# Performance work log

Measured on AMD Instinct MI355X. Metric: run time of the kernel, lower is better.

## Reference

```python
import jax, jax.numpy as jnp
import numpy as np


def setup_inputs() -> dict:
    key = jax.random.key(0)
    k1, k2, k3, k4 = jax.random.split(key, 4)
    d_in, d_out = 1024, 1024
    x = jax.random.normal(k1, (4, 2048, d_in), dtype=jnp.float32)
    # nn.Linear weights, stored as [d_in, d_out] for x @ W (torch stores transpose)
    s = 1.0 / np.sqrt(d_in)
    Wq = jax.random.normal(k2, (d_in, d_out), dtype=jnp.float32) * s
    Wk = jax.random.normal(k3, (d_in, d_out), dtype=jnp.float32) * s
    Wv = jax.random.normal(k4, (d_in, d_out), dtype=jnp.float32) * s
    return {"x": x, "Wq": Wq, "Wk": Wk, "Wv": Wv}


def reference(x, Wq, Wk, Wv):
    # x: [b, s, d_in]; projections (no bias)
    q = jnp.einsum('bsi,io->bso', x, Wq)
    k = jnp.einsum('bsi,io->bso', x, Wk)
    v = jnp.einsum('bsi,io->bso', x, Wv)
    d_out = k.shape[-1]
    scores = jnp.einsum('bqd,bkd->bqk', q, k) / jnp.sqrt(jnp.float32(d_out))
    seq_len = x.shape[1]
    causal = jnp.tril(jnp.ones((seq_len, seq_len), dtype=bool))  # [s, s]
    scores = jnp.where(causal[None, :, :], scores, -jnp.inf)
    weights = jax.nn.softmax(scores, axis=-1)
    return jnp.einsum('bqk,bkd->bqd', weights, v)
```

## Files before the change

### kernel.cpp

```cpp
#include <hip/hip_runtime.h>

typedef __attribute__((ext_vector_type(8))) short bf16x8;
typedef __attribute__((ext_vector_type(4))) float f32x4;
typedef unsigned int u32;

__device__ __forceinline__ unsigned short f2bf(float f) {
  union { float f; unsigned int u; } a; a.f = f;
  unsigned int u = a.u;
  u += 0x7FFFu + ((u >> 16) & 1u);
  return (unsigned short)(u >> 16);
}
__device__ __forceinline__ float bf2f(unsigned short h) {
  union { unsigned int u; float f; } a; a.u = ((unsigned int)h) << 16;
  return a.f;
}

__device__ __forceinline__ void gload16(const unsigned short* g, unsigned short* l) {
  __builtin_amdgcn_global_load_lds((const __attribute__((address_space(1))) u32*)g,
                                   (__attribute__((address_space(3))) u32*)l, 16, 0, 0);
}

#define TM 128
#define TN 128
#define BK 64

template<int MODE>
__global__ __launch_bounds__(256, 4)
void gemm_bt(const unsigned short* __restrict__ A,
             const unsigned short* __restrict__ Bm,
             float* __restrict__ Cf,
             unsigned short* __restrict__ Cb,
             int K, long aBatch, long bBatch, long cBatch, float scale)
{
  int z = blockIdx.z;
  A  += (long)z * aBatch;
  Bm += (long)z * bBatch;
  if (MODE == 2) Cb += (long)z * cBatch;
  if (MODE == 3) Cf += (long)z * cBatch;

  int bm, bn;
  if (MODE == 2) {
    int f = blockIdx.x;
    int r = (int)((sqrtf((float)(8 * f + 1)) - 1.0f) * 0.5f);
    while ((r + 1) * (r + 2) / 2 <= f) r++;
    while (r * (r + 1) / 2 > f) r--;
    bm = r * TM;
    bn = (f - r * (r + 1) / 2) * TN;
  } else if (MODE == 3) {
    bm = (15 - blockIdx.y) * TM;
    bn = blockIdx.x * TN;
  } else {
    bm = blockIdx.y * TM;
    bn = blockIdx.x * TN;
  }
  int Keff = (MODE == 3) ? (bm + TM) : K;

  __shared__ __align__(16) unsigned short As[TM * BK];
  __shared__ __align__(16) unsigned short Bs[TN * BK];

  int tid  = threadIdx.x;
  int wave = tid >> 6, lane = tid & 63;
  int wm = (wave >> 1) * 64, wn = (wave & 1) * 64;
  int quad = lane >> 4, l16 = lane & 15;

  int r8 = lane >> 3;
  int c  = (lane & 7) ^ r8;
  int rs = wave * 32 + r8;
  const unsigned short* Ag = A  + (long)(bm + rs) * K + c * 8;
  const unsigned short* Bg = Bm + (long)(bn + rs) * K + c * 8;
  unsigned short* Al = &As[(wave * 32) * BK];
  unsigned short* Bl = &Bs[(wave * 32) * BK];

  f32x4 acc[4][4] = {};

  for (int k0 = 0; k0 < Keff; k0 += BK) {
#pragma unroll
    for (int g = 0; g < 4; g++) {
      gload16(Ag + k0 + (long)g * 8 * K, Al + g * 8 * BK);
      gload16(Bg + k0 + (long)g * 8 * K, Bl + g * 8 * BK);
    }
    __syncthreads();

#pragma unroll
    for (int h = 0; h < 2; h++) {
      bf16x8 af[4], bfr[4];
#pragma unroll
      for (int i = 0; i < 4; i++)
        af[i]  = *(const bf16x8*)&As[(wm + i * 16 + l16) * BK + (((quad + 4 * h) ^ (l16 & 7)) * 8)];
#pragma unroll
      for (int j = 0; j < 4; j++)
        bfr[j] = *(const bf16x8*)&Bs[(wn + j * 16 + l16) * BK + (((quad + 4 * h) ^ (l16 & 7)) * 8)];
#pragma unroll
      for (int i = 0; i < 4; i++)
#pragma unroll
        for (int j = 0; j < 4; j++)
          acc[i][j] = __builtin_amdgcn_mfma_f32_16x16x32_bf16(af[i], bfr[j], acc[i][j], 0, 0, 0);
    }
    __syncthreads();
  }

#pragma unroll
  for (int i = 0; i < 4; i++) {
    int grow0 = bm + wm + i * 16 + quad * 4;
#pragma unroll
    for (int j = 0; j < 4; j++) {
      int gcol = bn + wn + j * 16 + l16;
      if (MODE == 0) {
        int which = gcol >> 10;
        int col = gcol & 1023;
        if (which < 2) {
          unsigned short* dst = Cb + (long)which * 8192 * 1024;
#pragma unroll
          for (int r = 0; r < 4; r++)
            dst[(long)(grow0 + r) * 1024 + col] = f2bf(acc[i][j][r]);
        } else {
          unsigned short* Vt = Cb + (long)2 * 8192 * 1024;
          int bb = grow0 >> 11, s = grow0 & 2047;
          ushort4 pk;
          pk.x = f2bf(acc[i][j][0]); pk.y = f2bf(acc[i][j][1]);
          pk.z = f2bf(acc[i][j][2]); pk.w = f2bf(acc[i][j][3]);
          *(ushort4*)(Vt + ((long)bb * 1024 + col) * 2048 + s) = pk;
        }
      } else if (MODE == 2) {
#pragma unroll
        for (int r = 0; r < 4; r++)
          Cb[(long)(grow0 + r) * 2048 + gcol] = f2bf(acc[i][j][r] * scale);
      } else {
#pragma unroll
        for (int r = 0; r < 4; r++)
          Cf[(long)(grow0 + r) * 1024 + gcol] = acc[i][j][r];
      }
    }
  }
}

__global__ __launch_bounds__(256)
void cvt_bf16(const float* __restrict__ in, unsigned short* __restrict__ out, long n)
{
  long i = ((long)blockIdx.x * 256 + threadIdx.x) * 4;
  if (i >= n) return;
  float4 v = *(const float4*)(in + i);
  ushort4 o;
  o.x = f2bf(v.x); o.y = f2bf(v.y); o.z = f2bf(v.z); o.w = f2bf(v.w);
  *(ushort4*)(out + i) = o;
}

__global__ __launch_bounds__(256)
void trans_cvt(const float* __restrict__ W0, const float* __restrict__ W1, const float* __restrict__ W2,
               unsigned short* __restrict__ T0, unsigned short* __restrict__ T1, unsigned short* __restrict__ T2)
{
  int z = blockIdx.z;
  const float* W   = (z == 0) ? W0 : (z == 1) ? W1 : W2;
  unsigned short* T = (z == 0) ? T0 : (z == 1) ? T1 : T2;
  __shared__ float tile[32][33];
  int kb = blockIdx.x * 32, nb = blockIdx.y * 32;
  int tx = threadIdx.x & 31, ty = threadIdx.x >> 5;
  for (int r = ty; r < 32; r += 8)
    tile[r][tx] = W[(long)(kb + r) * 1024 + nb + tx];
  __syncthreads();
  for (int r = ty; r < 32; r += 8)
    T[(long)(nb + r) * 1024 + kb + tx] = f2bf(tile[tx][r]);
}

__global__ __launch_bounds__(256)
void softmax_rows(const unsigned short* __restrict__ Sc, unsigned short* __restrict__ P)
{
  int row = blockIdx.x, b = blockIdx.y;
  const unsigned short* Sr = Sc + ((long)b * 2048 + row) * 2048;
  unsigned short* Pr = P + ((long)b * 2048 + row) * 2048;
  int n = row + 1;
  int tid = threadIdx.x;
  int wave = tid >> 6, lane = tid & 63;
  __shared__ float sh[2048];
  __shared__ float red[4];

  float lmax = -1e30f;
  for (int j0 = tid * 4; j0 < n; j0 += 1024) {
    ushort4 rw = *(const ushort4*)(Sr + j0);
    float4 v;
    v.x = (j0 + 0 < n) ? bf2f(rw.x) : -1e30f;
    v.y = (j0 + 1 < n) ? bf2f(rw.y) : -1e30f;
    v.z = (j0 + 2 < n) ? bf2f(rw.z) : -1e30f;
    v.w = (j0 + 3 < n) ? bf2f(rw.w) : -1e30f;
    *(float4*)(sh + j0) = v;
    lmax = fmaxf(fmaxf(v.x, v.y), fmaxf(fmaxf(v.z, v.w), lmax));
  }
  for (int off = 32; off; off >>= 1) lmax = fmaxf(lmax, __shfl_down(lmax, off));
  if (lane == 0) red[wave] = lmax;
  __syncthreads();
  float rmax = fmaxf(fmaxf(red[0], red[1]), fmaxf(red[2], red[3]));
  __syncthreads();

  float lsum = 0.f;
  for (int j0 = tid * 4; j0 < n; j0 += 1024) {
    float4 v = *(const float4*)(sh + j0);
    v.x = __expf(v.x - rmax); v.y = __expf(v.y - rmax);
    v.z = __expf(v.z - rmax); v.w = __expf(v.w - rmax);
    *(float4*)(sh + j0) = v;
    lsum += v.x + v.y + v.z + v.w;
  }
  for (int off = 32; off; off >>= 1) lsum += __shfl_down(lsum, off);
  if (lane == 0) red[wave] = lsum;
  __syncthreads();
  float rinv = 1.0f / (red[0] + red[1] + red[2] + red[3]);

  int nW = (n + 255) & ~255;
  for (int j0 = tid * 4; j0 < nW; j0 += 1024) {
    ushort4 o;
    if (j0 + 3 < n) {
      float4 v = *(const float4*)(sh + j0);
      o.x = f2bf(v.x * rinv); o.y = f2bf(v.y * rinv);
      o.z = f2bf(v.z * rinv); o.w = f2bf(v.w * rinv);
    } else {
      float4 v = *(const float4*)(sh + j0);
      o.x = (j0 + 0 < n) ? f2bf(v.x * rinv) : (unsigned short)0;
      o.y = (j0 + 1 < n) ? f2bf(v.y * rinv) : (unsigned short)0;
      o.z = (j0 + 2 < n) ? f2bf(v.z * rinv) : (unsigned short)0;
      o.w = (j0 + 3 < n) ? f2bf(v.w * rinv) : (unsigned short)0;
    }
    *(ushort4*)(Pr + j0) = o;
  }
}

extern "C" void kernel_launch(void* const* d_in, const int* in_sizes, int n_in,
                              void* d_out, int out_size, void* d_ws, size_t ws_size,
                              hipStream_t stream) {
  const float* x  = (const float*)d_in[0];
  const float* Wq = (const float*)d_in[1];
  const float* Wk = (const float*)d_in[2];
  const float* Wv = (const float*)d_in[3];
  float* out = (float*)d_out;

  unsigned short* Xb  = (unsigned short*)d_ws;
  unsigned short* WqT = Xb  + (long)8192 * 1024;
  unsigned short* Q   = WqT + (long)3072 * 1024;
  unsigned short* Kb  = Q   + (long)8192 * 1024;
  unsigned short* Vt  = Kb  + (long)8192 * 1024;
  unsigned short* Sc  = Vt  + (long)8192 * 1024;
  unsigned short* P   = Sc  + (long)4 * 2048 * 2048;
  unsigned short* WkT = WqT + (long)1024 * 1024;
  unsigned short* WvT = WkT + (long)1024 * 1024;

  cvt_bf16<<<8192, 256, 0, stream>>>(x, Xb, (long)8388608);
  trans_cvt<<<dim3(32, 32, 3), 256, 0, stream>>>(Wq, Wk, Wv, WqT, WkT, WvT);

  gemm_bt<0><<<dim3(24, 64, 1), 256, 0, stream>>>(Xb, WqT, nullptr, Q, 1024, 0, 0, 0, 1.f);

  gemm_bt<2><<<dim3(136, 1, 4), 256, 0, stream>>>(Q, Kb, nullptr, Sc, 1024,
      (long)2048 * 1024, (long)2048 * 1024, (long)2048 * 2048, 0.03125f);

  softmax_rows<<<dim3(2048, 4), 256, 0, stream>>>(Sc, P);

  gemm_bt<3><<<dim3(8, 16, 4), 256, 0, stream>>>(P, Vt, out, nullptr, 2048,
      (long)2048 * 2048, (long)1024 * 2048, (long)2048 * 1024, 1.f);
}
```

Before: 246.7 us.

## Fuse exp and row-sum into QK GEMM epilogue, split-K long rows in PV

Removes the separate softmax pass. The QK^T GEMM epilogue now writes exp(score*scale) with the causal mask applied and atomically adds per-row sums into a buffer. The max subtraction is skipped, on the assumption that scores stay small enough not to overflow. The PV GEMM splits the K range for the bottom half of the row tiles into two blocks to balance work, with the second block writing to a separate buffer. A finalize kernel adds the partial result and divides by the row sum. This trades the softmax kernel's read and write of the score matrix for atomics, an extra fp32 partial buffer and an extra pass over the output.

```diff
diff --git a/kernel.cpp b/kernel.cpp
--- a/kernel.cpp
+++ b/kernel.cpp
@@ -29,16 +29,18 @@
 void gemm_bt(const unsigned short* __restrict__ A,
              const unsigned short* __restrict__ Bm,
              float* __restrict__ Cf,
+             float* __restrict__ Cf2,
              unsigned short* __restrict__ Cb,
              int K, long aBatch, long bBatch, long cBatch, float scale)
 {
   int z = blockIdx.z;
   A  += (long)z * aBatch;
   Bm += (long)z * bBatch;
-  if (MODE == 2) Cb += (long)z * cBatch;
-  if (MODE == 3) Cf += (long)z * cBatch;
-
-  int bm, bn;
+  if (MODE == 2) { Cb += (long)z * cBatch; Cf += (long)z * 2048; }
+  if (MODE == 3) { Cf += (long)z * cBatch; Cf2 += (long)z * 1024 * 1024; }
+
+  int bm, bn, kStart = 0, kEnd;
+  bool toMain = true;
   if (MODE == 2) {
     int f = blockIdx.x;
     int r = (int)((sqrtf((float)(8 * f + 1)) - 1.0f) * 0.5f);
@@ -46,14 +48,26 @@
     while (r * (r + 1) / 2 > f) r--;
     bm = r * TM;
     bn = (f - r * (r + 1) / 2) * TN;
+    kEnd = K;
   } else if (MODE == 3) {
-    bm = (15 - blockIdx.y) * TM;
+    int yy = blockIdx.y;
+    if (yy < 16) {
+      int s = 15 - yy;
+      bm = s * TM;
+      kEnd = (s < 8) ? 128 * (s + 1) : 64 * (s + 1);
+    } else {
+      int s = yy - 8;
+      bm = s * TM;
+      kStart = 64 * (s + 1);
+      kEnd = 128 * (s + 1);
+      toMain = false;
+    }
     bn = blockIdx.x * TN;
   } else {
     bm = blockIdx.y * TM;
     bn = blockIdx.x * TN;
-  }
-  int Keff = (MODE == 3) ? (bm + TM) : K;
+    kEnd = K;
+  }
 
   __shared__ __align__(16) unsigned short As[TM * BK];
   __shared__ __align__(16) unsigned short Bs[TN * BK];
@@ -73,7 +87,7 @@
 
   f32x4 acc[4][4] = {};
 
-  for (int k0 = 0; k0 < Keff; k0 += BK) {
+  for (int k0 = kStart; k0 < kEnd; k0 += BK) {
 #pragma unroll
     for (int g = 0; g < 4; g++) {
       gload16(Ag + k0 + (long)g * 8 * K, Al + g * 8 * BK);
@@ -102,33 +116,55 @@
 #pragma unroll
   for (int i = 0; i < 4; i++) {
     int grow0 = bm + wm + i * 16 + quad * 4;
-#pragma unroll
-    for (int j = 0; j < 4; j++) {
-      int gcol = bn + wn + j * 16 + l16;
-      if (MODE == 0) {
-        int which = gcol >> 10;
-        int col = gcol & 1023;
-        if (which < 2) {
-          unsigned short* dst = Cb + (long)which * 8192 * 1024;
-#pragma unroll
-          for (int r = 0; r < 4; r++)
-            dst[(long)(grow0 + r) * 1024 + col] = f2bf(acc[i][j][r]);
+    if (MODE == 2) {
+#pragma unroll
+      for (int r = 0; r < 4; r++) {
+        int grow = grow0 + r;
+        float rowpart = 0.f;
+#pragma unroll
+        for (int j = 0; j < 4; j++) {
+          int gcol = bn + wn + j * 16 + l16;
+          float e = (gcol <= grow) ? __expf(acc[i][j][r] * scale) : 0.f;
+          rowpart += e;
+          Cb[(long)grow * 2048 + gcol] = f2bf(e);
+        }
+        rowpart += __shfl_xor(rowpart, 1);
+        rowpart += __shfl_xor(rowpart, 2);
+        rowpart += __shfl_xor(rowpart, 4);
+        rowpart += __shfl_xor(rowpart, 8);
+        if (l16 == 0) atomicAdd(&Cf[grow], rowpart);
+      }
+    } else {
+#pragma unroll
+      for (int j = 0; j < 4; j++) {
+        int gcol = bn + wn + j * 16 + l16;
+        if (MODE == 0) {
+          int which = gcol >> 10;
+          int col = gcol & 1023;
+          if (which < 2) {
+            unsigned short* dst = Cb + (long)which * 8192 * 1024;
+#pragma unroll
+            for (int r = 0; r < 4; r++)
+              dst[(long)(grow0 + r) * 1024 + col] = f2bf(acc[i][j][r]);
+          } else {
+            unsigned short* Vt = Cb + (long)2 * 8192 * 1024;
+            int bb = grow0 >> 11, s = grow0 & 2047;
+            ushort4 pk;
+            pk.x = f2bf(acc[i][j][0]); pk.y = f2bf(acc[i][j][1]);
+            pk.z = f2bf(acc[i][j][2]); pk.w = f2bf(acc[i][j][3]);
+            *(ushort4*)(Vt + ((long)bb * 1024 + col) * 2048 + s) = pk;
+          }
         } else {
-          unsigned short* Vt = Cb + (long)2 * 8192 * 1024;
-          int bb = grow0 >> 11, s = grow0 & 2047;
-          ushort4 pk;
-          pk.x = f2bf(acc[i][j][0]); pk.y = f2bf(acc[i][j][1]);
-          pk.z = f2bf(acc[i][j][2]); pk.w = f2bf(acc[i][j][3]);
-          *(ushort4*)(Vt + ((long)bb * 1024 + col) * 2048 + s) = pk;
+          if (toMain) {
+#pragma unroll
+            for (int r = 0; r < 4; r++)
+              Cf[(long)(grow0 + r) * 1024 + gcol] = acc[i][j][r];
+          } else {
+#pragma unroll
+            for (int r = 0; r < 4; r++)
+              Cf2[(long)(grow0 + r - 1024) * 1024 + gcol] = acc[i][j][r];
+          }
         }
-      } else if (MODE == 2) {
-#pragma unroll
-        for (int r = 0; r < 4; r++)
-          Cb[(long)(grow0 + r) * 2048 + gcol] = f2bf(acc[i][j][r] * scale);
-      } else {
-#pragma unroll
-        for (int r = 0; r < 4; r++)
-          Cf[(long)(grow0 + r) * 1024 + gcol] = acc[i][j][r];
       }
     }
   }
@@ -143,6 +179,14 @@
   ushort4 o;
   o.x = f2bf(v.x); o.y = f2bf(v.y); o.z = f2bf(v.z); o.w = f2bf(v.w);
   *(ushort4*)(out + i) = o;
+}
+
+__global__ __launch_bounds__(256)
+void zero_rsum(float* __restrict__ rsum)
+{
+  long i = ((long)blockIdx.x * 256 + threadIdx.x) * 4;
+  float4 zz = {0.f, 0.f, 0.f, 0.f};
+  *(float4*)(rsum + i) = zz;
 }
 
 __global__ __launch_bounds__(256)
@@ -163,63 +207,20 @@
 }
 
 __global__ __launch_bounds__(256)
-void softmax_rows(const unsigned short* __restrict__ Sc, unsigned short* __restrict__ P)
-{
-  int row = blockIdx.x, b = blockIdx.y;
-  const unsigned short* Sr = Sc + ((long)b * 2048 + row) * 2048;
-  unsigned short* Pr = P + ((long)b * 2048 + row) * 2048;
-  int n = row + 1;
-  int tid = threadIdx.x;
-  int wave = tid >> 6, lane = tid & 63;
-  __shared__ float sh[2048];
-  __shared__ float red[4];
-
-  float lmax = -1e30f;
-  for (int j0 = tid * 4; j0 < n; j0 += 1024) {
-    ushort4 rw = *(const ushort4*)(Sr + j0);
-    float4 v;
-    v.x = (j0 + 0 < n) ? bf2f(rw.x) : -1e30f;
-    v.y = (j0 + 1 < n) ? bf2f(rw.y) : -1e30f;
-    v.z = (j0 + 2 < n) ? bf2f(rw.z) : -1e30f;
-    v.w = (j0 + 3 < n) ? bf2f(rw.w) : -1e30f;
-    *(float4*)(sh + j0) = v;
-    lmax = fmaxf(fmaxf(v.x, v.y), fmaxf(fmaxf(v.z, v.w), lmax));
-  }
-  for (int off = 32; off; off >>= 1) lmax = fmaxf(lmax, __shfl_down(lmax, off));
-  if (lane == 0) red[wave] = lmax;
-  __syncthreads();
-  float rmax = fmaxf(fmaxf(red[0], red[1]), fmaxf(red[2], red[3]));
-  __syncthreads();
-
-  float lsum = 0.f;
-  for (int j0 = tid * 4; j0 < n; j0 += 1024) {
-    float4 v = *(const float4*)(sh + j0);
-    v.x = __expf(v.x - rmax); v.y = __expf(v.y - rmax);
-    v.z = __expf(v.z - rmax); v.w = __expf(v.w - rmax);
-    *(float4*)(sh + j0) = v;
-    lsum += v.x + v.y + v.z + v.w;
-  }
-  for (int off = 32; off; off >>= 1) lsum += __shfl_down(lsum, off);
-  if (lane == 0) red[wave] = lsum;
-  __syncthreads();
-  float rinv = 1.0f / (red[0] + red[1] + red[2] + red[3]);
-
-  int nW = (n + 255) & ~255;
-  for (int j0 = tid * 4; j0 < nW; j0 += 1024) {
-    ushort4 o;
-    if (j0 + 3 < n) {
-      float4 v = *(const float4*)(sh + j0);
-      o.x = f2bf(v.x * rinv); o.y = f2bf(v.y * rinv);
-      o.z = f2bf(v.z * rinv); o.w = f2bf(v.w * rinv);
-    } else {
-      float4 v = *(const float4*)(sh + j0);
-      o.x = (j0 + 0 < n) ? f2bf(v.x * rinv) : (unsigned short)0;
-      o.y = (j0 + 1 < n) ? f2bf(v.y * rinv) : (unsigned short)0;
-      o.z = (j0 + 2 < n) ? f2bf(v.z * rinv) : (unsigned short)0;
-      o.w = (j0 + 3 < n) ? f2bf(v.w * rinv) : (unsigned short)0;
-    }
-    *(ushort4*)(Pr + j0) = o;
-  }
+void finalize(float* __restrict__ out, const float* __restrict__ O2,
+              const float* __restrict__ rsum)
+{
+  int r = blockIdx.x, b = blockIdx.y;
+  float rinv = 1.0f / rsum[(long)b * 2048 + r];
+  long o = (((long)b * 2048 + r) * 1024) + threadIdx.x * 4;
+  float4 v = *(const float4*)(out + o);
+  if (r >= 1024) {
+    long o2 = (((long)b * 1024 + (r - 1024)) * 1024) + threadIdx.x * 4;
+    float4 w = *(const float4*)(O2 + o2);
+    v.x += w.x; v.y += w.y; v.z += w.z; v.w += w.w;
+  }
+  v.x *= rinv; v.y *= rinv; v.z *= rinv; v.w *= rinv;
+  *(float4*)(out + o) = v;
 }
 
 extern "C" void kernel_launch(void* const* d_in, const int* in_sizes, int n_in,
@@ -236,21 +237,24 @@
   unsigned short* Q   = WqT + (long)3072 * 1024;
   unsigned short* Kb  = Q   + (long)8192 * 1024;
   unsigned short* Vt  = Kb  + (long)8192 * 1024;
-  unsigned short* Sc  = Vt  + (long)8192 * 1024;
-  unsigned short* P   = Sc  + (long)4 * 2048 * 2048;
+  unsigned short* E   = Vt  + (long)8192 * 1024;
+  float* O2           = (float*)(E + (long)4 * 2048 * 2048);
+  float* rsum         = O2 + (long)4 * 1024 * 1024;
   unsigned short* WkT = WqT + (long)1024 * 1024;
   unsigned short* WvT = WkT + (long)1024 * 1024;
 
   cvt_bf16<<<8192, 256, 0, stream>>>(x, Xb, (long)8388608);
   trans_cvt<<<dim3(32, 32, 3), 256, 0, stream>>>(Wq, Wk, Wv, WqT, WkT, WvT);
-
-  gemm_bt<0><<<dim3(24, 64, 1), 256, 0, stream>>>(Xb, WqT, nullptr, Q, 1024, 0, 0, 0, 1.f);
-
-  gemm_bt<2><<<dim3(136, 1, 4), 256, 0, stream>>>(Q, Kb, nullptr, Sc, 1024,
+  zero_rsum<<<8, 256, 0, stream>>>(rsum);
+
+  gemm_bt<0><<<dim3(24, 64, 1), 256, 0, stream>>>(Xb, WqT, nullptr, nullptr, Q,
+      1024, 0, 0, 0, 1.f);
+
+  gemm_bt<2><<<dim3(136, 1, 4), 256, 0, stream>>>(Q, Kb, rsum, nullptr, E, 1024,
       (long)2048 * 1024, (long)2048 * 1024, (long)2048 * 2048, 0.03125f);
 
-  softmax_rows<<<dim3(2048, 4), 256, 0, stream>>>(Sc, P);
-
-  gemm_bt<3><<<dim3(8, 16, 4), 256, 0, stream>>>(P, Vt, out, nullptr, 2048,
+  gemm_bt<3><<<dim3(8, 24, 4), 256, 0, stream>>>(E, Vt, out, O2, nullptr, 2048,
       (long)2048 * 2048, (long)1024 * 2048, (long)2048 * 1024, 1.f);
-}
+
+  finalize<<<dim3(2048, 4), 256, 0, stream>>>(out, O2, rsum);
+}
```

After: 243.4 us. No clear change (-1.3%).
